# Kernel optimization log

Measured on AMD Instinct MI355X. Metric: run time of the kernel, lower is better.

## Reference

```python
import jax, jax.numpy as jnp
import numpy as np

N_NODES = 50000
N_FEATURES = 128
HIDDEN = 64
N_EDGES = 1600000


def gcn_conv(x, src, dst, edge_w, W, b, num_nodes):
    """torch_geometric GCNConv with edge weights: add self-loops (weight 1),
    symmetric deg^-1/2 normalization, aggregate into dst, then bias."""
    loop = jnp.arange(num_nodes)
    src_f = jnp.concatenate([src, loop])
    dst_f = jnp.concatenate([dst, loop])
    w_f = jnp.concatenate([edge_w, jnp.ones((num_nodes,), dtype=edge_w.dtype)])
    deg = jax.ops.segment_sum(w_f, dst_f, num_segments=num_nodes)
    dinv = jnp.where(deg > 0, jax.lax.rsqrt(deg), 0.0)
    norm = dinv[src_f] * w_f * dinv[dst_f]            # [E+N]
    h = x @ W                                          # [N, out]
    msg = h[src_f] * norm[:, None]                     # [E+N, out]
    out = jax.ops.segment_sum(msg, dst_f, num_segments=num_nodes)
    return out + b


def setup_inputs() -> dict:
    key = jax.random.key(0)
    ks = jax.random.split(key, 12)
    features = jax.random.normal(ks[0], (N_NODES, N_FEATURES), dtype=jnp.float32)
    edge_index = jax.random.randint(ks[1], (2, N_EDGES), 0, N_NODES, dtype=jnp.int64)
    edge_attr = jax.random.uniform(ks[2], (N_EDGES,), dtype=jnp.float32)
    s = 0.05
    W1 = jax.random.normal(ks[3], (N_FEATURES, HIDDEN), dtype=jnp.float32) * s
    b1 = jnp.zeros((HIDDEN,), dtype=jnp.float32)
    W2 = jax.random.normal(ks[4], (HIDDEN, HIDDEN // 2), dtype=jnp.float32) * s
    b2 = jnp.zeros((HIDDEN // 2,), dtype=jnp.float32)
    Wd = jax.random.normal(ks[5], (N_FEATURES, 2), dtype=jnp.float32) * s
    bd = jnp.zeros((2,), dtype=jnp.float32)
    w_fc = jax.random.normal(ks[6], (N_NODES * 2,), dtype=jnp.float32) * s
    b_fc = jnp.zeros((), dtype=jnp.float32)
    return {"features": features, "edge_index": edge_index, "edge_attr": edge_attr,
            "W1": W1, "b1": b1, "W2": W2, "b2": b2, "Wd": Wd, "bd": bd,
            "w_fc": w_fc, "b_fc": b_fc}


def reference(features, edge_index, edge_attr, W1, b1, W2, b2, Wd, bd, w_fc, b_fc):
    N = features.shape[0]
    src, dst = edge_index[0], edge_index[1]
    # --- generator encoder (GAE.encode): GCN -> relu -> GCN -> tanh ---
    h = gcn_conv(features, src, dst, edge_attr, W1, b1, N)
    h = jax.nn.relu(h)                                  # dropout inactive (eval)
    z = jnp.tanh(gcn_conv(h, src, dst, edge_attr, W2, b2, N))  # [N, HIDDEN//2]
    # --- residual path: tile z to n_features width and add input features ---
    rep = features.shape[1] // z.shape[1]
    x = jnp.tile(z, (1, rep)) + features                # [N, n_features]
    # (edge_probabilities = z@z.T + rebuilt adjacency is computed by the
    #  generator but discarded by GraphCounteRGAN.forward -> dead code)
    # --- discriminator: GCN -> relu -> flatten -> fc -> sigmoid ---
    d = jax.nn.relu(gcn_conv(x, src, dst, edge_attr, Wd, bd, N))  # [N, 2]
    logit = jnp.dot(d.reshape(-1), w_fc) + b_fc
    return jax.nn.sigmoid(logit)
```

## Files before the change

kernel.cpp:

```cpp
#include <hip/hip_runtime.h>
#include <math.h>

#define BLK 256
#define CHUNK 4096
#define BSH 9
#define BNODES 512
#define MAXNB 128

__device__ __forceinline__ unsigned short f2bf(float f) {
    unsigned u = __float_as_uint(f);
    u += 0x7FFFu + ((u >> 16) & 1u);
    return (unsigned short)(u >> 16);
}
__device__ __forceinline__ float bf2f(unsigned short b) {
    return __uint_as_float(((unsigned)b) << 16);
}

__global__ void detect_kernel(const int* __restrict__ idx, int E,
                              int* __restrict__ flag, float* __restrict__ acc) {
    int t = threadIdx.x;
    long long j = (long long)t * (E / 64);
    int hi = idx[2 * j + 1];
    unsigned long long b = __ballot(hi != 0);
    if (t == 0) { *flag = (b == 0ULL) ? 1 : 0; *acc = 0.f; }
}

__global__ __launch_bounds__(256) void bucket_hist_kernel(const int* __restrict__ idx,
                                                          const int* __restrict__ flag,
                                                          int* __restrict__ blockCnt,
                                                          int E, int NB) {
    __shared__ int hist[MAXNB];
    int t = threadIdx.x;
    if (t < NB) hist[t] = 0;
    __syncthreads();
    bool i64 = (*flag) != 0;
    int e0 = blockIdx.x * CHUNK;
    int e1 = min(e0 + CHUNK, E);
    for (int e = e0 + t; e < e1; e += 256) {
        int d = i64 ? idx[2 * (E + e)] : idx[E + e];
        atomicAdd(&hist[d >> BSH], 1);
    }
    __syncthreads();
    if (t < NB) blockCnt[blockIdx.x * NB + t] = hist[t];
}

__global__ __launch_bounds__(256) void col_scan_kernel(const int* __restrict__ blockCnt,
                                                       int* __restrict__ blockBase,
                                                       int* __restrict__ bucketTotal,
                                                       int NBLK, int NB) {
    __shared__ int s[256];
    __shared__ int carry;
    int bkt = blockIdx.x;
    int t = threadIdx.x;
    if (t == 0) carry = 0;
    __syncthreads();
    for (int base = 0; base < NBLK; base += 256) {
        int i = base + t;
        int v = (i < NBLK) ? blockCnt[i * NB + bkt] : 0;
        s[t] = v;
        __syncthreads();
        for (int off = 1; off < 256; off <<= 1) {
            int x = (t >= off) ? s[t - off] : 0;
            __syncthreads();
            s[t] += x;
            __syncthreads();
        }
        if (i < NBLK) blockBase[i * NB + bkt] = carry + s[t] - v;
        __syncthreads();
        if (t == 0) carry += s[255];
        __syncthreads();
    }
    if (t == 0) bucketTotal[bkt] = carry;
}

__global__ void bucket_scan_kernel(const int* __restrict__ bucketTotal,
                                   int* __restrict__ bucketBase, int NB) {
    __shared__ int s[128];
    int t = threadIdx.x;
    int v = (t < NB) ? bucketTotal[t] : 0;
    s[t] = v;
    __syncthreads();
    for (int off = 1; off < 128; off <<= 1) {
        int x = (t >= off) ? s[t - off] : 0;
        __syncthreads();
        s[t] += x;
        __syncthreads();
    }
    if (t < NB) bucketBase[t] = s[t] - v;
}

__global__ __launch_bounds__(256) void bucket_scatter_kernel(const int* __restrict__ idx,
                                                             const float* __restrict__ ew,
                                                             const int* __restrict__ flag,
                                                             const int* __restrict__ bucketBase,
                                                             const int* __restrict__ blockBase,
                                                             int2* __restrict__ temp,
                                                             int E, int NB) {
    __shared__ int base[MAXNB];
    __shared__ int fill[MAXNB];
    int t = threadIdx.x;
    if (t < NB) {
        base[t] = bucketBase[t] + blockBase[blockIdx.x * NB + t];
        fill[t] = 0;
    }
    __syncthreads();
    bool i64 = (*flag) != 0;
    int e0 = blockIdx.x * CHUNK;
    int e1 = min(e0 + CHUNK, E);
    for (int e = e0 + t; e < e1; e += 256) {
        int s_, d;
        if (i64) { s_ = idx[2 * e]; d = idx[2 * (E + e)]; }
        else     { s_ = idx[e];     d = idx[E + e]; }
        float w = ew[e];
        int b = d >> BSH;
        int pos = base[b] + atomicAdd(&fill[b], 1);
        temp[pos] = make_int2(s_ | ((d & (BNODES - 1)) << 16), __float_as_int(w));
    }
}

__global__ __launch_bounds__(1024) void csr_build_kernel(const int2* __restrict__ temp,
                                                         const int* __restrict__ bucketBase,
                                                         unsigned* __restrict__ csrw,
                                                         int* __restrict__ row,
                                                         float* __restrict__ dinv,
                                                         int N, int NB, int E) {
    __shared__ int cnt[BNODES];
    __shared__ float dw[BNODES];
    __shared__ int offs[BNODES];
    int bkt = blockIdx.x;
    int t = threadIdx.x;
    int node0 = bkt << BSH;
    int nn = min(BNODES, N - node0);
    for (int i = t; i < BNODES; i += 1024) { cnt[i] = 0; dw[i] = 0.f; }
    __syncthreads();
    int p0 = bucketBase[bkt];
    int p1 = (bkt + 1 < NB) ? bucketBase[bkt + 1] : E;
    for (int p = p0 + t; p < p1; p += 1024) {
        int2 v = temp[p];
        int dl = (v.x >> 16) & (BNODES - 1);
        atomicAdd(&cnt[dl], 1);
        atomicAdd(&dw[dl], __int_as_float(v.y));
    }
    __syncthreads();
    int v = 0;
    if (t < BNODES) { v = cnt[t]; offs[t] = v; }
    __syncthreads();
    for (int off = 1; off < BNODES; off <<= 1) {
        int x = 0;
        if (t < BNODES && t >= off) x = offs[t - off];
        __syncthreads();
        if (t < BNODES) offs[t] += x;
        __syncthreads();
    }
    if (t < BNODES) {
        int excl = offs[t] - v;
        if (t < nn) {
            row[node0 + t] = p0 + excl;
            dinv[node0 + t] = rsqrtf(1.f + dw[t]);
        }
        offs[t] = excl;
    }
    if (bkt == NB - 1 && t == 0) row[N] = E;
    __syncthreads();
    for (int i = t; i < BNODES; i += 1024) cnt[i] = 0;
    __syncthreads();
    for (int p = p0 + t; p < p1; p += 1024) {
        int2 v2 = temp[p];
        int dl = (v2.x >> 16) & (BNODES - 1);
        int pos = p0 + offs[dl] + atomicAdd(&cnt[dl], 1);
        unsigned wb = (unsigned)v2.y;
        wb += 0x7FFFu + ((wb >> 16) & 1u);
        csrw[pos] = ((unsigned)v2.x & 0xFFFFu) | (wb & 0xFFFF0000u);
    }
}

__global__ void norm_kernel(unsigned* __restrict__ csrw, const float* __restrict__ dinv, int E) {
    int e = blockIdx.x * BLK + threadIdx.x;
    if (e >= E) return;
    unsigned pe = csrw[e];
    float w = __uint_as_float(pe & 0xFFFF0000u) * dinv[pe & 0xFFFFu];
    unsigned wb = __float_as_uint(w);
    wb += 0x7FFFu + ((wb >> 16) & 1u);
    csrw[e] = (pe & 0xFFFFu) | (wb & 0xFFFF0000u);
}

__global__ __launch_bounds__(256) void gather64_kernel(const int* __restrict__ row,
                                                       const unsigned* __restrict__ csrw,
                                                       const unsigned short* __restrict__ h,
                                                       const float* __restrict__ dinv,
                                                       const float* __restrict__ bias,
                                                       float* __restrict__ out, int N) {
    int wid = (blockIdx.x * 256 + threadIdx.x) >> 6;
    int o = threadIdx.x & 63;
    if (wid >= N) return;
    float di = dinv[wid];
    int p0 = row[wid], p1 = row[wid + 1];
    const unsigned short* hb = h + o;
    float es0 = 0.f, es1 = 0.f;
    for (int p = p0; p < p1; p += 64) {
        int q = p + o;
        unsigned pe = (q < p1) ? csrw[q] : 0u;
        int m = min(64, p1 - p);
        int mp = (m + 7) & ~7;
        for (int j = 0; j < mp; j += 8) {
            unsigned e0 = (unsigned)__shfl((int)pe, j + 0, 64);
            unsigned e1 = (unsigned)__shfl((int)pe, j + 1, 64);
            unsigned e2 = (unsigned)__shfl((int)pe, j + 2, 64);
            unsigned e3 = (unsigned)__shfl((int)pe, j + 3, 64);
            unsigned e4 = (unsigned)__shfl((int)pe, j + 4, 64);
            unsigned e5 = (unsigned)__shfl((int)pe, j + 5, 64);
            unsigned e6 = (unsigned)__shfl((int)pe, j + 6, 64);
            unsigned e7 = (unsigned)__shfl((int)pe, j + 7, 64);
            float h0 = bf2f(hb[(e0 & 0xFFFFu) * 64]);
            float h1 = bf2f(hb[(e1 & 0xFFFFu) * 64]);
            float h2 = bf2f(hb[(e2 & 0xFFFFu) * 64]);
            float h3 = bf2f(hb[(e3 & 0xFFFFu) * 64]);
            float h4 = bf2f(hb[(e4 & 0xFFFFu) * 64]);
            float h5 = bf2f(hb[(e5 & 0xFFFFu) * 64]);
            float h6 = bf2f(hb[(e6 & 0xFFFFu) * 64]);
            float h7 = bf2f(hb[(e7 & 0xFFFFu) * 64]);
            es0 = fmaf(__uint_as_float(e0 & 0xFFFF0000u), h0, es0);
            es1 = fmaf(__uint_as_float(e1 & 0xFFFF0000u), h1, es1);
            es0 = fmaf(__uint_as_float(e2 & 0xFFFF0000u), h2, es0);
            es1 = fmaf(__uint_as_float(e3 & 0xFFFF0000u), h3, es1);
            es0 = fmaf(__uint_as_float(e4 & 0xFFFF0000u), h4, es0);
            es1 = fmaf(__uint_as_float(e5 & 0xFFFF0000u), h5, es1);
            es0 = fmaf(__uint_as_float(e6 & 0xFFFF0000u), h6, es0);
            es1 = fmaf(__uint_as_float(e7 & 0xFFFF0000u), h7, es1);
        }
    }
    out[wid * 64 + o] = bias[o] + di * (di * bf2f(h[(size_t)wid * 64 + o]) + es0 + es1);
}

__global__ __launch_bounds__(256) void gather32_kernel(const int* __restrict__ row,
                                                       const unsigned* __restrict__ csrw,
                                                       const unsigned short* __restrict__ h,
                                                       const float* __restrict__ dinv,
                                                       const float* __restrict__ bias,
                                                       float* __restrict__ out, int N) {
    int wid = (blockIdx.x * 256 + threadIdx.x) >> 6;
    int lane = threadIdx.x & 63;
    int o = lane & 31;
    int g = lane >> 5;
    if (wid >= N) return;
    float di = dinv[wid];
    int p0 = row[wid], p1 = row[wid + 1];
    const unsigned short* hb = h + o;
    float es0 = 0.f, es1 = 0.f;
    for (int p = p0; p < p1; p += 64) {
        int q = p + lane;
        unsigned pe = (q < p1) ? csrw[q] : 0u;
        int m = min(64, p1 - p);
        int mp = (m + 7) & ~7;
        for (int j = g; j < mp; j += 8) {
            unsigned e0 = (unsigned)__shfl((int)pe, j + 0, 64);
            unsigned e1 = (unsigned)__shfl((int)pe, j + 2, 64);
            unsigned e2 = (unsigned)__shfl((int)pe, j + 4, 64);
            unsigned e3 = (unsigned)__shfl((int)pe, j + 6, 64);
            float h0 = bf2f(hb[(e0 & 0xFFFFu) * 32]);
            float h1 = bf2f(hb[(e1 & 0xFFFFu) * 32]);
            float h2 = bf2f(hb[(e2 & 0xFFFFu) * 32]);
            float h3 = bf2f(hb[(e3 & 0xFFFFu) * 32]);
            es0 = fmaf(__uint_as_float(e0 & 0xFFFF0000u), h0, es0);
            es1 = fmaf(__uint_as_float(e1 & 0xFFFF0000u), h1, es1);
            es0 = fmaf(__uint_as_float(e2 & 0xFFFF0000u), h2, es0);
            es1 = fmaf(__uint_as_float(e3 & 0xFFFF0000u), h3, es1);
        }
    }
    float es = es0 + es1;
    es += __shfl_down(es, 32, 64);
    if (g == 0) out[wid * 32 + o] = bias[o] + di * (di * bf2f(h[wid * 32 + o]) + es);
}

__global__ __launch_bounds__(256) void gather2_kernel(const int* __restrict__ row,
                                                      const unsigned* __restrict__ csrw,
                                                      const unsigned short* __restrict__ h,
                                                      const float* __restrict__ dinv,
                                                      const float* __restrict__ bias,
                                                      float* __restrict__ out, int N) {
    const unsigned* hp = (const unsigned*)h;
    int wid = (blockIdx.x * 256 + threadIdx.x) >> 6;
    int lane = threadIdx.x & 63;
    if (wid >= N) return;
    float di = dinv[wid];
    int p0 = row[wid], p1 = row[wid + 1];
    float a0 = 0.f, a1 = 0.f, b0 = 0.f, b1 = 0.f;
    int p = p0 + lane;
    for (; p + 64 < p1; p += 128) {
        unsigned pe0 = csrw[p];
        unsigned pe1 = csrw[p + 64];
        unsigned hw0 = hp[pe0 & 0xFFFFu];
        unsigned hw1 = hp[pe1 & 0xFFFFu];
        float w0 = __uint_as_float(pe0 & 0xFFFF0000u);
        float w1 = __uint_as_float(pe1 & 0xFFFF0000u);
        a0 = fmaf(w0, __uint_as_float(hw0 << 16), a0);
        a1 = fmaf(w0, __uint_as_float(hw0 & 0xFFFF0000u), a1);
        b0 = fmaf(w1, __uint_as_float(hw1 << 16), b0);
        b1 = fmaf(w1, __uint_as_float(hw1 & 0xFFFF0000u), b1);
    }
    if (p < p1) {
        unsigned pe0 = csrw[p];
        unsigned hw0 = hp[pe0 & 0xFFFFu];
        float w0 = __uint_as_float(pe0 & 0xFFFF0000u);
        a0 = fmaf(w0, __uint_as_float(hw0 << 16), a0);
        a1 = fmaf(w0, __uint_as_float(hw0 & 0xFFFF0000u), a1);
    }
    a0 += b0; a1 += b1;
#pragma unroll
    for (int off = 32; off > 0; off >>= 1) {
        a0 += __shfl_down(a0, off, 64);
        a1 += __shfl_down(a1, off, 64);
    }
    if (lane == 0) {
        unsigned hw = hp[wid];
        out[wid * 2 + 0] = bias[0] + di * (di * __uint_as_float(hw << 16) + a0);
        out[wid * 2 + 1] = bias[1] + di * (di * __uint_as_float(hw & 0xFFFF0000u) + a1);
    }
}

__global__ __launch_bounds__(256) void mm1_kernel(const float* __restrict__ X,
                                                  const float* __restrict__ W,
                                                  unsigned short* __restrict__ Y, int N) {
    __shared__ float Xs[16 * 132];
    __shared__ float4 Ws[128 * 16];
    const float4* Wg = (const float4*)W;
    for (int i = threadIdx.x; i < 128 * 16; i += 256) Ws[i] = Wg[i];
    int row0 = blockIdx.x * 16;
    for (int i = threadIdx.x; i < 16 * 128; i += 256) {
        int r = i >> 7, k = i & 127;
        int row = row0 + r;
        Xs[r * 132 + k] = (row < N) ? X[row * 128 + k] : 0.f;
    }
    __syncthreads();
    int r = threadIdx.x >> 4;
    int c4 = threadIdx.x & 15;
    int row = row0 + r;
    float4 acc = {0.f, 0.f, 0.f, 0.f};
#pragma unroll 4
    for (int k = 0; k < 128; ++k) {
        float xv = Xs[r * 132 + k];
        float4 wv = Ws[k * 16 + c4];
        acc.x = fmaf(xv, wv.x, acc.x);
        acc.y = fmaf(xv, wv.y, acc.y);
        acc.z = fmaf(xv, wv.z, acc.z);
        acc.w = fmaf(xv, wv.w, acc.w);
    }
    if (row < N) {
        ushort4 o;
        o.x = f2bf(acc.x); o.y = f2bf(acc.y); o.z = f2bf(acc.z); o.w = f2bf(acc.w);
        ((ushort4*)Y)[row * 16 + c4] = o;
    }
}

__global__ __launch_bounds__(256) void mm2_kernel(const float* __restrict__ H,
                                                  const float* __restrict__ W,
                                                  unsigned short* __restrict__ Y, int N) {
    __shared__ float Xs[32 * 68];
    __shared__ float4 Ws[64 * 8];
    const float4* Wg = (const float4*)W;
    for (int i = threadIdx.x; i < 64 * 8; i += 256) Ws[i] = Wg[i];
    int row0 = blockIdx.x * 32;
    for (int i = threadIdx.x; i < 32 * 64; i += 256) {
        int r = i >> 6, k = i & 63;
        int row = row0 + r;
        Xs[r * 68 + k] = (row < N) ? fmaxf(H[row * 64 + k], 0.f) : 0.f;
    }
    __syncthreads();
    int r = threadIdx.x >> 3;
    int c4 = threadIdx.x & 7;
    int row = row0 + r;
    float4 acc = {0.f, 0.f, 0.f, 0.f};
#pragma unroll 4
    for (int k = 0; k < 64; ++k) {
        float xv = Xs[r * 68 + k];
        float4 wv = Ws[k * 8 + c4];
        acc.x = fmaf(xv, wv.x, acc.x);
        acc.y = fmaf(xv, wv.y, acc.y);
        acc.z = fmaf(xv, wv.z, acc.z);
        acc.w = fmaf(xv, wv.w, acc.w);
    }
    if (row < N) {
        ushort4 o;
        o.x = f2bf(acc.x); o.y = f2bf(acc.y); o.z = f2bf(acc.z); o.w = f2bf(acc.w);
        ((ushort4*)Y)[row * 8 + c4] = o;
    }
}

__global__ __launch_bounds__(256) void disc_mm_kernel(const float* __restrict__ Z,
                                                      const float* __restrict__ F,
                                                      const float* __restrict__ Wd,
                                                      unsigned short* __restrict__ Y, int N) {
    __shared__ float Ws[256];
    if (threadIdx.x < 256) Ws[threadIdx.x] = Wd[threadIdx.x];
    __syncthreads();
    int n = blockIdx.x * 256 + threadIdx.x;
    if (n >= N) return;
    float zt[32];
#pragma unroll
    for (int j = 0; j < 32; ++j) zt[j] = tanhf(Z[n * 32 + j]);
    float a0 = 0.f, a1 = 0.f;
    const float* fr = F + (size_t)n * 128;
#pragma unroll 4
    for (int c = 0; c < 128; ++c) {
        float xv = zt[c & 31] + fr[c];
        a0 = fmaf(xv, Ws[c * 2 + 0], a0);
        a1 = fmaf(xv, Ws[c * 2 + 1], a1);
    }
    ushort2 o;
    o.x = f2bf(a0); o.y = f2bf(a1);
    ((ushort2*)Y)[n] = o;
}

__global__ void init_deg_kernel(float* __restrict__ deg, int N) {
    int n = blockIdx.x * BLK + threadIdx.x;
    if (n < N) deg[n] = 1.0f;
}

__global__ void edge_deg_kernel(const int* __restrict__ idx, const float* __restrict__ ew,
                                const int* __restrict__ flag, float* __restrict__ deg, int E) {
    int e = blockIdx.x * BLK + threadIdx.x;
    if (e >= E) return;
    int d = (*flag) ? idx[2 * (E + e)] : idx[E + e];
    atomicAdd(&deg[d], ew[e]);
}

__global__ void dinv_kernel(float* __restrict__ deg, int N) {
    int n = blockIdx.x * BLK + threadIdx.x;
    if (n < N) deg[n] = rsqrtf(deg[n]);
}

template <int WD>
__global__ void init_agg_kernel(const unsigned short* __restrict__ h, const float* __restrict__ dinv,
                                const float* __restrict__ bias, float* __restrict__ agg, int N) {
    int i = blockIdx.x * BLK + threadIdx.x;
    if (i >= N * WD) return;
    int n = i / WD, o = i % WD;
    float di = dinv[n];
    agg[i] = bias[o] + di * di * bf2f(h[i]);
}

template <int WD>
__global__ void edge_agg_kernel(const int* __restrict__ idx, const float* __restrict__ ew,
                                const int* __restrict__ flag, const float* __restrict__ dinv,
                                const unsigned short* __restrict__ h, float* __restrict__ agg, int E) {
    int gid = blockIdx.x * BLK + threadIdx.x;
    if (gid >= E * WD) return;
    int e = gid / WD;
    int o = gid % WD;
    int s, d;
    if (*flag) { s = idx[2 * e]; d = idx[2 * (E + e)]; }
    else       { s = idx[e];     d = idx[E + e]; }
    float nrm = dinv[s] * ew[e] * dinv[d];
    atomicAdd(&agg[d * WD + o], nrm * bf2f(h[s * WD + o]));
}

__global__ void reduce_kernel(const float* __restrict__ dmat, const float* __restrict__ wfc,
                              float* __restrict__ acc, int M) {
    int i = blockIdx.x * BLK + threadIdx.x;
    float v = 0.f;
    if (i < M) v = fmaxf(dmat[i], 0.f) * wfc[i];
#pragma unroll
    for (int off = 32; off > 0; off >>= 1) v += __shfl_down(v, off, 64);
    if ((threadIdx.x & 63) == 0) atomicAdd(acc, v);
}

__global__ void final_kernel(const float* __restrict__ acc, const float* __restrict__ bfc,
                             float* __restrict__ out) {
    float x = *acc + *bfc;
    out[0] = 1.f / (1.f + expf(-x));
}

extern "C" void kernel_launch(void* const* d_in, const int* in_sizes, int n_in,
                              void* d_out, int out_size, void* d_ws, size_t ws_size,
                              hipStream_t stream) {
    const float* feat = (const float*)d_in[0];
    const int*   eidx = (const int*)d_in[1];
    const float* ew   = (const float*)d_in[2];
    const float* W1   = (const float*)d_in[3];
    const float* b1   = (const float*)d_in[4];
    const float* W2   = (const float*)d_in[5];
    const float* b2   = (const float*)d_in[6];
    const float* Wd   = (const float*)d_in[7];
    const float* bd   = (const float*)d_in[8];
    const float* wfc  = (const float*)d_in[9];
    const float* bfc  = (const float*)d_in[10];

    const int N = in_sizes[0] / 128;
    const int E = in_sizes[2];

    const int NB   = (N + BNODES - 1) >> BSH;
    const int NBLK = (E + CHUNK - 1) / CHUNK;

    float* ws = (float*)d_ws;
    size_t u = 0;
    float* dinv = ws + u; u += N;
    if (u & 1) u++;
    size_t M1 = ((size_t)N * 32 > (size_t)E * 2) ? (size_t)N * 32 : (size_t)E * 2;
    unsigned short* h = (unsigned short*)(ws + u); int2* temp = (int2*)h; u += M1;
    if (u & 1) u++;
    float* agg = ws + u; u += (size_t)N * 64;
    float* acc = ws + u; u += 1;
    int* flag = (int*)(ws + u); u += 1;
    int* row  = (int*)(ws + u); u += (size_t)N + 1;
    int* bucketTotal = (int*)(ws + u); u += NB;
    int* bucketBase  = (int*)(ws + u); u += NB + 1;
    int* blockCnt    = (int*)(ws + u); u += (size_t)NBLK * NB;
    int* blockBase   = (int*)(ws + u); u += (size_t)NBLK * NB;
    unsigned* csrw   = (unsigned*)(ws + u); u += (size_t)E;
    size_t need = u * 4;

    float* out = (float*)d_out;

    const int gN = (N + BLK - 1) / BLK;
    const int gE = (E + BLK - 1) / BLK;
    const int gW = (N + 3) / 4;

    if (ws_size >= need && N <= 65536 && NB <= MAXNB) {
        hipLaunchKernelGGL(detect_kernel, dim3(1), dim3(64), 0, stream, eidx, E, flag, acc);
        hipLaunchKernelGGL(bucket_hist_kernel, dim3(NBLK), dim3(256), 0, stream,
                           eidx, flag, blockCnt, E, NB);
        hipLaunchKernelGGL(col_scan_kernel, dim3(NB), dim3(256), 0, stream,
                           blockCnt, blockBase, bucketTotal, NBLK, NB);
        hipLaunchKernelGGL(bucket_scan_kernel, dim3(1), dim3(128), 0, stream,
                           bucketTotal, bucketBase, NB);
        hipLaunchKernelGGL(bucket_scatter_kernel, dim3(NBLK), dim3(256), 0, stream,
                           eidx, ew, flag, bucketBase, blockBase, temp, E, NB);
        hipLaunchKernelGGL(csr_build_kernel, dim3(NB), dim3(1024), 0, stream,
                           temp, bucketBase, csrw, row, dinv, N, NB, E);
        hipLaunchKernelGGL(norm_kernel, dim3(gE), dim3(BLK), 0, stream, csrw, dinv, E);

        hipLaunchKernelGGL(mm1_kernel, dim3((N + 15) / 16), dim3(256), 0, stream, feat, W1, h, N);
        hipLaunchKernelGGL(gather64_kernel, dim3(gW), dim3(256), 0, stream,
                           row, csrw, h, dinv, b1, agg, N);
        hipLaunchKernelGGL(mm2_kernel, dim3((N + 31) / 32), dim3(256), 0, stream, agg, W2, h, N);
        hipLaunchKernelGGL(gather32_kernel, dim3(gW), dim3(256), 0, stream,
                           row, csrw, h, dinv, b2, agg, N);
        hipLaunchKernelGGL(disc_mm_kernel, dim3((N + 255) / 256), dim3(256), 0, stream,
                           agg, feat, Wd, h, N);
        hipLaunchKernelGGL(gather2_kernel, dim3(gW), dim3(256), 0, stream,
                           row, csrw, h, dinv, bd, agg, N);
    } else {
        hipLaunchKernelGGL(detect_kernel, dim3(1), dim3(64), 0, stream, eidx, E, flag, acc);
        hipLaunchKernelGGL(init_deg_kernel, dim3(gN), dim3(BLK), 0, stream, dinv, N);
        hipLaunchKernelGGL(edge_deg_kernel, dim3(gE), dim3(BLK), 0, stream, eidx, ew, flag, dinv, E);
        hipLaunchKernelGGL(dinv_kernel, dim3(gN), dim3(BLK), 0, stream, dinv, N);

        hipLaunchKernelGGL(mm1_kernel, dim3((N + 15) / 16), dim3(256), 0, stream, feat, W1, h, N);
        hipLaunchKernelGGL((init_agg_kernel<64>), dim3((N * 64 + BLK - 1) / BLK), dim3(BLK), 0, stream,
                           h, dinv, b1, agg, N);
        hipLaunchKernelGGL((edge_agg_kernel<64>), dim3((E / BLK) * 64 + 64), dim3(BLK), 0, stream,
                           eidx, ew, flag, dinv, h, agg, E);
        hipLaunchKernelGGL(mm2_kernel, dim3((N + 31) / 32), dim3(256), 0, stream, agg, W2, h, N);
        hipLaunchKernelGGL((init_agg_kernel<32>), dim3((N * 32 + BLK - 1) / BLK), dim3(BLK), 0, stream,
                           h, dinv, b2, agg, N);
        hipLaunchKernelGGL((edge_agg_kernel<32>), dim3((E / BLK) * 32 + 32), dim3(BLK), 0, stream,
                           eidx, ew, flag, dinv, h, agg, E);
        hipLaunchKernelGGL(disc_mm_kernel, dim3((N + 255) / 256), dim3(256), 0, stream,
                           agg, feat, Wd, h, N);
        hipLaunchKernelGGL((init_agg_kernel<2>), dim3((N * 2 + BLK - 1) / BLK), dim3(BLK), 0, stream,
                           h, dinv, bd, agg, N);
        hipLaunchKernelGGL((edge_agg_kernel<2>), dim3((E * 2 + BLK - 1) / BLK), dim3(BLK), 0, stream,
                           eidx, ew, flag, dinv, h, agg, E);
    }

    hipLaunchKernelGGL(reduce_kernel, dim3((N * 2 + BLK - 1) / BLK), dim3(BLK), 0, stream,
                       agg, wfc, acc, N * 2);
    hipLaunchKernelGGL(final_kernel, dim3(1), dim3(1), 0, stream, acc, bfc, out);
}
```

Measured before the change: 322.3 us.

## Use smaller CSR buckets and register-block mm1 with bf16 weights

```diff
diff --git a/kernel.cpp b/kernel.cpp
--- a/kernel.cpp
+++ b/kernel.cpp
@@ -3,9 +3,9 @@
 
 #define BLK 256
 #define CHUNK 4096
-#define BSH 9
-#define BNODES 512
-#define MAXNB 128
+#define BSH 7
+#define BNODES 128
+#define MAXNB 512
 
 __device__ __forceinline__ unsigned short f2bf(float f) {
     unsigned u = __float_as_uint(f);
@@ -31,7 +31,7 @@
                                                           int E, int NB) {
     __shared__ int hist[MAXNB];
     int t = threadIdx.x;
-    if (t < NB) hist[t] = 0;
+    for (int i = t; i < NB; i += 256) hist[i] = 0;
     __syncthreads();
     bool i64 = (*flag) != 0;
     int e0 = blockIdx.x * CHUNK;
@@ -41,7 +41,7 @@
         atomicAdd(&hist[d >> BSH], 1);
     }
     __syncthreads();
-    if (t < NB) blockCnt[blockIdx.x * NB + t] = hist[t];
+    for (int i = t; i < NB; i += 256) blockCnt[blockIdx.x * NB + i] = hist[i];
 }
 
 __global__ __launch_bounds__(256) void col_scan_kernel(const int* __restrict__ blockCnt,
@@ -73,14 +73,14 @@
     if (t == 0) bucketTotal[bkt] = carry;
 }
 
-__global__ void bucket_scan_kernel(const int* __restrict__ bucketTotal,
-                                   int* __restrict__ bucketBase, int NB) {
-    __shared__ int s[128];
+__global__ __launch_bounds__(512) void bucket_scan_kernel(const int* __restrict__ bucketTotal,
+                                                          int* __restrict__ bucketBase, int NB) {
+    __shared__ int s[512];
     int t = threadIdx.x;
     int v = (t < NB) ? bucketTotal[t] : 0;
     s[t] = v;
     __syncthreads();
-    for (int off = 1; off < 128; off <<= 1) {
+    for (int off = 1; off < 512; off <<= 1) {
         int x = (t >= off) ? s[t - off] : 0;
         __syncthreads();
         s[t] += x;
@@ -99,9 +99,9 @@
     __shared__ int base[MAXNB];
     __shared__ int fill[MAXNB];
     int t = threadIdx.x;
-    if (t < NB) {
-        base[t] = bucketBase[t] + blockBase[blockIdx.x * NB + t];
-        fill[t] = 0;
+    for (int i = t; i < NB; i += 256) {
+        base[i] = bucketBase[i] + blockBase[blockIdx.x * NB + i];
+        fill[i] = 0;
     }
     __syncthreads();
     bool i64 = (*flag) != 0;
@@ -118,12 +118,12 @@
     }
 }
 
-__global__ __launch_bounds__(1024) void csr_build_kernel(const int2* __restrict__ temp,
-                                                         const int* __restrict__ bucketBase,
-                                                         unsigned* __restrict__ csrw,
-                                                         int* __restrict__ row,
-                                                         float* __restrict__ dinv,
-                                                         int N, int NB, int E) {
+__global__ __launch_bounds__(512) void csr_build_kernel(const int2* __restrict__ temp,
+                                                        const int* __restrict__ bucketBase,
+                                                        unsigned* __restrict__ csrw,
+                                                        int* __restrict__ row,
+                                                        float* __restrict__ dinv,
+                                                        int N, int NB, int E) {
     __shared__ int cnt[BNODES];
     __shared__ float dw[BNODES];
     __shared__ int offs[BNODES];
@@ -131,11 +131,11 @@
     int t = threadIdx.x;
     int node0 = bkt << BSH;
     int nn = min(BNODES, N - node0);
-    for (int i = t; i < BNODES; i += 1024) { cnt[i] = 0; dw[i] = 0.f; }
+    if (t < BNODES) { cnt[t] = 0; dw[t] = 0.f; }
     __syncthreads();
     int p0 = bucketBase[bkt];
     int p1 = (bkt + 1 < NB) ? bucketBase[bkt + 1] : E;
-    for (int p = p0 + t; p < p1; p += 1024) {
+    for (int p = p0 + t; p < p1; p += 512) {
         int2 v = temp[p];
         int dl = (v.x >> 16) & (BNODES - 1);
         atomicAdd(&cnt[dl], 1);
@@ -162,9 +162,9 @@
     }
     if (bkt == NB - 1 && t == 0) row[N] = E;
     __syncthreads();
-    for (int i = t; i < BNODES; i += 1024) cnt[i] = 0;
-    __syncthreads();
-    for (int p = p0 + t; p < p1; p += 1024) {
+    if (t < BNODES) cnt[t] = 0;
+    __syncthreads();
+    for (int p = p0 + t; p < p1; p += 512) {
         int2 v2 = temp[p];
         int dl = (v2.x >> 16) & (BNODES - 1);
         int pos = p0 + offs[dl] + atomicAdd(&cnt[dl], 1);
@@ -321,34 +321,50 @@
 __global__ __launch_bounds__(256) void mm1_kernel(const float* __restrict__ X,
                                                   const float* __restrict__ W,
                                                   unsigned short* __restrict__ Y, int N) {
-    __shared__ float Xs[16 * 132];
-    __shared__ float4 Ws[128 * 16];
+    __shared__ float Xs[32 * 132];
+    __shared__ uint2 Wsb[128 * 16];
     const float4* Wg = (const float4*)W;
-    for (int i = threadIdx.x; i < 128 * 16; i += 256) Ws[i] = Wg[i];
-    int row0 = blockIdx.x * 16;
-    for (int i = threadIdx.x; i < 16 * 128; i += 256) {
+    for (int i = threadIdx.x; i < 128 * 16; i += 256) {
+        float4 wv = Wg[i];
+        unsigned lo = ((unsigned)f2bf(wv.x)) | (((unsigned)f2bf(wv.y)) << 16);
+        unsigned hi = ((unsigned)f2bf(wv.z)) | (((unsigned)f2bf(wv.w)) << 16);
+        Wsb[i] = make_uint2(lo, hi);
+    }
+    int row0 = blockIdx.x * 32;
+    for (int i = threadIdx.x; i < 32 * 128; i += 256) {
         int r = i >> 7, k = i & 127;
-        int row = row0 + r;
-        Xs[r * 132 + k] = (row < N) ? X[row * 128 + k] : 0.f;
-    }
-    __syncthreads();
-    int r = threadIdx.x >> 4;
+        int rr = row0 + r;
+        Xs[r * 132 + k] = (rr < N) ? X[(size_t)rr * 128 + k] : 0.f;
+    }
+    __syncthreads();
+    int r0 = (threadIdx.x >> 4) * 2;
     int c4 = threadIdx.x & 15;
-    int row = row0 + r;
-    float4 acc = {0.f, 0.f, 0.f, 0.f};
+    float4 a0 = {0.f, 0.f, 0.f, 0.f};
+    float4 a1 = {0.f, 0.f, 0.f, 0.f};
 #pragma unroll 4
     for (int k = 0; k < 128; ++k) {
-        float xv = Xs[r * 132 + k];
-        float4 wv = Ws[k * 16 + c4];
-        acc.x = fmaf(xv, wv.x, acc.x);
-        acc.y = fmaf(xv, wv.y, acc.y);
-        acc.z = fmaf(xv, wv.z, acc.z);
-        acc.w = fmaf(xv, wv.w, acc.w);
-    }
+        float x0 = Xs[r0 * 132 + k];
+        float x1 = Xs[(r0 + 1) * 132 + k];
+        uint2 wp = Wsb[k * 16 + c4];
+        float w0 = __uint_as_float(wp.x << 16);
+        float w1 = __uint_as_float(wp.x & 0xFFFF0000u);
+        float w2 = __uint_as_float(wp.y << 16);
+        float w3 = __uint_as_float(wp.y & 0xFFFF0000u);
+        a0.x = fmaf(x0, w0, a0.x); a0.y = fmaf(x0, w1, a0.y);
+        a0.z = fmaf(x0, w2, a0.z); a0.w = fmaf(x0, w3, a0.w);
+        a1.x = fmaf(x1, w0, a1.x); a1.y = fmaf(x1, w1, a1.y);
+        a1.z = fmaf(x1, w2, a1.z); a1.w = fmaf(x1, w3, a1.w);
+    }
+    int row = row0 + r0;
     if (row < N) {
         ushort4 o;
-        o.x = f2bf(acc.x); o.y = f2bf(acc.y); o.z = f2bf(acc.z); o.w = f2bf(acc.w);
-        ((ushort4*)Y)[row * 16 + c4] = o;
+        o.x = f2bf(a0.x); o.y = f2bf(a0.y); o.z = f2bf(a0.z); o.w = f2bf(a0.w);
+        ((ushort4*)Y)[(size_t)row * 16 + c4] = o;
+    }
+    if (row + 1 < N) {
+        ushort4 o;
+        o.x = f2bf(a1.x); o.y = f2bf(a1.y); o.z = f2bf(a1.z); o.w = f2bf(a1.w);
+        ((ushort4*)Y)[(size_t)(row + 1) * 16 + c4] = o;
     }
 }
 
@@ -521,15 +537,15 @@
                            eidx, flag, blockCnt, E, NB);
         hipLaunchKernelGGL(col_scan_kernel, dim3(NB), dim3(256), 0, stream,
                            blockCnt, blockBase, bucketTotal, NBLK, NB);
-        hipLaunchKernelGGL(bucket_scan_kernel, dim3(1), dim3(128), 0, stream,
+        hipLaunchKernelGGL(bucket_scan_kernel, dim3(1), dim3(512), 0, stream,
                            bucketTotal, bucketBase, NB);
         hipLaunchKernelGGL(bucket_scatter_kernel, dim3(NBLK), dim3(256), 0, stream,
                            eidx, ew, flag, bucketBase, blockBase, temp, E, NB);
-        hipLaunchKernelGGL(csr_build_kernel, dim3(NB), dim3(1024), 0, stream,
+        hipLaunchKernelGGL(csr_build_kernel, dim3(NB), dim3(512), 0, stream,
                            temp, bucketBase, csrw, row, dinv, N, NB, E);
         hipLaunchKernelGGL(norm_kernel, dim3(gE), dim3(BLK), 0, stream, csrw, dinv, E);
 
-        hipLaunchKernelGGL(mm1_kernel, dim3((N + 15) / 16), dim3(256), 0, stream, feat, W1, h, N);
+        hipLaunchKernelGGL(mm1_kernel, dim3((N + 31) / 32), dim3(256), 0, stream, feat, W1, h, N);
         hipLaunchKernelGGL(gather64_kernel, dim3(gW), dim3(256), 0, stream,
                            row, csrw, h, dinv, b1, agg, N);
         hipLaunchKernelGGL(mm2_kernel, dim3((N + 31) / 32), dim3(256), 0, stream, agg, W2, h, N);
@@ -545,7 +561,7 @@
         hipLaunchKernelGGL(edge_deg_kernel, dim3(gE), dim3(BLK), 0, stream, eidx, ew, flag, dinv, E);
         hipLaunchKernelGGL(dinv_kernel, dim3(gN), dim3(BLK), 0, stream, dinv, N);
 
-        hipLaunchKernelGGL(mm1_kernel, dim3((N + 15) / 16), dim3(256), 0, stream, feat, W1, h, N);
+        hipLaunchKernelGGL(mm1_kernel, dim3((N + 31) / 32), dim3(256), 0, stream, feat, W1, h, N);
         hipLaunchKernelGGL((init_agg_kernel<64>), dim3((N * 64 + BLK - 1) / BLK), dim3(BLK), 0, stream,
                            h, dinv, b1, agg, N);
         hipLaunchKernelGGL((edge_agg_kernel<64>), dim3((E / BLK) * 64 + 64), dim3(BLK), 0, stream,
```

Result: faster. 310.6 us (-3.6%).
